# Kernel tuning notes

Hardware: AMD Instinct MI355X
Metric: run time of the kernel (lower is better)

## Reference

```python
import jax, jax.numpy as jnp
import numpy as np

N_NODES = 100000
N_EDGES = 1600000
D_IN = 128
D_OUT = 128


def setup_inputs() -> dict:
    key = jax.random.key(0)
    ks = jax.random.split(key, 6)
    x = jax.random.normal(ks[0], (N_NODES, D_IN), dtype=jnp.float32)
    edge_index = jax.random.randint(ks[1], (2, N_EDGES), 0, N_NODES, dtype=jnp.int64)
    W_l = jax.random.normal(ks[2], (D_OUT, D_IN), dtype=jnp.float32) * 0.05
    b_l = jax.random.normal(ks[3], (D_OUT,), dtype=jnp.float32) * 0.05
    W_r = jax.random.normal(ks[4], (D_OUT, D_IN), dtype=jnp.float32) * 0.05
    b_r = jax.random.normal(ks[5], (D_OUT,), dtype=jnp.float32) * 0.05
    return {"x": x, "edge_index": edge_index, "W_l": W_l, "b_l": b_l, "W_r": W_r, "b_r": b_r}


def reference(x, edge_index, W_l, b_l, W_r, b_r):
    # spmm(edge_index, x, reduce='mean'): out[row] = mean_{edges with that row} x[col]
    row = edge_index[0]
    col = edge_index[1]
    n = x.shape[0]
    agg = jax.ops.segment_sum(x[col], row, num_segments=n)  # [N, D_IN]
    deg = jax.ops.segment_sum(jnp.ones((edge_index.shape[1],), dtype=x.dtype), row, num_segments=n)
    mean = agg / jnp.maximum(deg, 1.0)[:, None]
    # lin_l(mean) + lin_r(x)
    return mean @ W_l.T + b_l + x @ W_r.T + b_r
```

## Files before the change

### kernel.cpp

```cpp
#include <hip/hip_runtime.h>

#define D 128
#define NPB 128
#define MAXBK 800
#define NBLK 256

typedef __attribute__((ext_vector_type(8))) short short8;
typedef __attribute__((ext_vector_type(4))) float f32x4;

__device__ __forceinline__ unsigned short f2bf(float f) {
    unsigned u = __float_as_uint(f);
    return (unsigned short)((u + 0x7fffu + ((u >> 16) & 1u)) >> 16);
}

__global__ void split_kernel(const float4* __restrict__ x, uint2* __restrict__ xh,
                             uint2* __restrict__ xl, int n4) {
    int i = blockIdx.x * blockDim.x + threadIdx.x;
    if (i >= n4) return;
    float4 v = x[i];
    unsigned short h0 = f2bf(v.x), h1 = f2bf(v.y), h2 = f2bf(v.z), h3 = f2bf(v.w);
    float r0 = v.x - __uint_as_float((unsigned)h0 << 16);
    float r1 = v.y - __uint_as_float((unsigned)h1 << 16);
    float r2 = v.z - __uint_as_float((unsigned)h2 << 16);
    float r3 = v.w - __uint_as_float((unsigned)h3 << 16);
    unsigned short l0 = f2bf(r0), l1 = f2bf(r1), l2 = f2bf(r2), l3 = f2bf(r3);
    uint2 hh, ll;
    hh.x = (unsigned)h0 | ((unsigned)h1 << 16);
    hh.y = (unsigned)h2 | ((unsigned)h3 << 16);
    ll.x = (unsigned)l0 | ((unsigned)l1 << 16);
    ll.y = (unsigned)l2 | ((unsigned)l3 << 16);
    xh[i] = hh;
    xl[i] = ll;
}

__global__ void prepw_kernel(const float* __restrict__ Wl_in, const float* __restrict__ bl,
                             const float* __restrict__ Wr_in, const float* __restrict__ br,
                             unsigned short* __restrict__ wh, unsigned short* __restrict__ wl,
                             float* __restrict__ bias) {
    int t = blockIdx.x * blockDim.x + threadIdx.x;
    if (t < 2 * D * D) {
        int n = t >> 7;
        int k = t & (D - 1);
        float v = (n < D) ? Wl_in[n * D + k] : Wr_in[(n - D) * D + k];
        unsigned short h = f2bf(v);
        float r = v - __uint_as_float((unsigned)h << 16);
        wh[t] = h;
        wl[t] = f2bf(r);
    }
    if (t < D) bias[t] = bl[t] + br[t];
}

__global__ __launch_bounds__(256) void hist_kernel(const int* __restrict__ ei,
                                                   int* __restrict__ cnt,
                                                   int E, int nbk, int chunk) {
    __shared__ int h[MAXBK];
    int b = blockIdx.x, t = threadIdx.x;
    for (int i = t; i < nbk; i += 256) h[i] = 0;
    __syncthreads();
    int lo = b * chunk, hi = min(E, lo + chunk);
    for (int e = lo + t; e < hi; e += 256)
        atomicAdd(&h[ei[e] >> 7], 1);
    __syncthreads();
    for (int i = t; i < nbk; i += 256) cnt[i * NBLK + b] = h[i];
}

__global__ __launch_bounds__(256) void scan_cnt_kernel(int* __restrict__ cnt,
                                                       int* __restrict__ btot) {
    int b = blockIdx.x, t = threadIdx.x;
    int lane = t & 63, w = t >> 6;
    int v = cnt[b * NBLK + t];
    int s = v;
    for (int off = 1; off < 64; off <<= 1) {
        int u = __shfl_up(s, off, 64);
        if (lane >= off) s += u;
    }
    __shared__ int wsum[4], woff[4];
    if (lane == 63) wsum[w] = s;
    __syncthreads();
    if (t == 0) {
        int run = 0;
        for (int i = 0; i < 4; ++i) { woff[i] = run; run += wsum[i]; }
        btot[b] = run;
    }
    __syncthreads();
    cnt[b * NBLK + t] = s - v + woff[w];
}

__global__ void scan_btot_kernel(const int* __restrict__ btot, int* __restrict__ bbase,
                                 int* __restrict__ row_start, int nbk, int n) {
    __shared__ int s[1024];
    int t = threadIdx.x;
    int v = (t < nbk) ? btot[t] : 0;
    s[t] = v;
    __syncthreads();
    for (int off = 1; off < 1024; off <<= 1) {
        int u = (t >= off) ? s[t - off] : 0;
        __syncthreads();
        s[t] += u;
        __syncthreads();
    }
    if (t < nbk) bbase[t] = s[t] - v;
    if (t == 1023) { bbase[nbk] = s[1023]; row_start[n] = s[1023]; }
}

__global__ __launch_bounds__(256) void scatter_kernel(const int* __restrict__ ei,
                                                      const int* __restrict__ cnt,
                                                      const int* __restrict__ bbase,
                                                      unsigned* __restrict__ pk,
                                                      int E, int nbk, int chunk) {
    __shared__ int curs[MAXBK];
    int b = blockIdx.x, t = threadIdx.x;
    for (int i = t; i < nbk; i += 256) curs[i] = bbase[i] + cnt[i * NBLK + b];
    __syncthreads();
    int lo = b * chunk, hi = min(E, lo + chunk);
    for (int e = lo + t; e < hi; e += 256) {
        int r = ei[e];
        int c = ei[E + e];
        int pos = atomicAdd(&curs[r >> 7], 1);
        pk[pos] = ((unsigned)(r & (NPB - 1)) << 17) | (unsigned)c;
    }
}

__global__ __launch_bounds__(256) void place_kernel(const int* __restrict__ bbase,
                                                    const unsigned* __restrict__ pk,
                                                    int* __restrict__ row_start,
                                                    int* __restrict__ col_sorted, int n) {
    __shared__ int hist[NPB];
    __shared__ int pre[NPB];
    int b = blockIdx.x, t = threadIdx.x;
    if (t < NPB) hist[t] = 0;
    __syncthreads();
    int s0 = bbase[b], e0 = bbase[b + 1];
    for (int i = s0 + t; i < e0; i += 256)
        atomicAdd(&hist[pk[i] >> 17], 1);
    __syncthreads();
    if (t < NPB) pre[t] = hist[t];
    __syncthreads();
    for (int off = 1; off < NPB; off <<= 1) {
        int u = (t >= off && t < NPB) ? pre[t - off] : 0;
        __syncthreads();
        if (t < NPB) pre[t] += u;
        __syncthreads();
    }
    if (t < NPB) {
        int ex = pre[t] - hist[t];
        int node = b * NPB + t;
        if (node < n) row_start[node] = s0 + ex;
        hist[t] = ex;
    }
    __syncthreads();
    for (int i = s0 + t; i < e0; i += 256) {
        unsigned p = pk[i];
        int slot = atomicAdd(&hist[p >> 17], 1);
        col_sorted[s0 + slot] = (int)(p & 0x1FFFFu);
    }
}

__global__ __launch_bounds__(256) void mm_kernel(const unsigned short* __restrict__ xh,
                                                 const unsigned short* __restrict__ xl,
                                                 const unsigned short* __restrict__ wh,
                                                 const unsigned short* __restrict__ wl,
                                                 const float* __restrict__ bias,
                                                 unsigned short* __restrict__ yl,
                                                 float* __restrict__ out, int n) {
    int w = threadIdx.x >> 6;
    int l = threadIdx.x & 63;
    int ml = l & 15;
    int kq = l >> 4;
    int m0 = blockIdx.x * 64;
    int n0 = w * 64;

    f32x4 acc[4][4];
#pragma unroll
    for (int a = 0; a < 4; ++a)
#pragma unroll
        for (int b = 0; b < 4; ++b) acc[a][b] = (f32x4){0.f, 0.f, 0.f, 0.f};

#pragma unroll
    for (int ks = 0; ks < 4; ++ks) {
        short8 Ah[4], Al[4];
#pragma unroll
        for (int mf = 0; mf < 4; ++mf) {
            int row = m0 + mf * 16 + ml;
            if (row > n - 1) row = n - 1;
            size_t off = (size_t)row * D + ks * 32 + kq * 8;
            Ah[mf] = *(const short8*)(xh + off);
            Al[mf] = *(const short8*)(xl + off);
        }
#pragma unroll
        for (int nf = 0; nf < 4; ++nf) {
            size_t boff = (size_t)(n0 + nf * 16 + ml) * D + ks * 32 + kq * 8;
            short8 Bh = *(const short8*)(wh + boff);
            short8 Bl = *(const short8*)(wl + boff);
#pragma unroll
            for (int mf = 0; mf < 4; ++mf) {
                acc[mf][nf] = __builtin_amdgcn_mfma_f32_16x16x32_bf16(Ah[mf], Bh, acc[mf][nf], 0, 0, 0);
                acc[mf][nf] = __builtin_amdgcn_mfma_f32_16x16x32_bf16(Ah[mf], Bl, acc[mf][nf], 0, 0, 0);
                acc[mf][nf] = __builtin_amdgcn_mfma_f32_16x16x32_bf16(Al[mf], Bh, acc[mf][nf], 0, 0, 0);
            }
        }
    }

    if (n0 < D) {
#pragma unroll
        for (int nf = 0; nf < 4; ++nf) {
            int col = n0 + nf * 16 + ml;
#pragma unroll
            for (int mf = 0; mf < 4; ++mf) {
                int rbase = m0 + mf * 16 + kq * 4;
#pragma unroll
                for (int r = 0; r < 4; ++r) {
                    int row = rbase + r;
                    if (row < n) yl[(size_t)row * D + col] = f2bf(acc[mf][nf][r]);
                }
            }
        }
    } else {
#pragma unroll
        for (int nf = 0; nf < 4; ++nf) {
            int col = n0 - D + nf * 16 + ml;
            float bv = bias[col];
#pragma unroll
            for (int mf = 0; mf < 4; ++mf) {
                int rbase = m0 + mf * 16 + kq * 4;
#pragma unroll
                for (int r = 0; r < 4; ++r) {
                    int row = rbase + r;
                    if (row < n) out[(size_t)row * D + col] = acc[mf][nf][r] + bv;
                }
            }
        }
    }
}

__global__ void gather_kernel(const unsigned short* __restrict__ yl,
                              const int* __restrict__ col_sorted,
                              const int* __restrict__ row_start,
                              float* __restrict__ out, int n) {
    int wave = (int)((blockIdx.x * (size_t)blockDim.x + threadIdx.x) >> 6);
    int lane = threadIdx.x & 63;
    if (wave >= n) return;
    int s = row_start[wave];
    int e = row_start[wave + 1];
    float a0 = 0.f, a1 = 0.f;
    int j = s;
    for (; j + 3 < e; j += 4) {
        int c0 = col_sorted[j], c1 = col_sorted[j + 1], c2 = col_sorted[j + 2], c3 = col_sorted[j + 3];
        unsigned v0 = *(const unsigned*)(yl + (size_t)c0 * D + 2 * lane);
        unsigned v1 = *(const unsigned*)(yl + (size_t)c1 * D + 2 * lane);
        unsigned v2 = *(const unsigned*)(yl + (size_t)c2 * D + 2 * lane);
        unsigned v3 = *(const unsigned*)(yl + (size_t)c3 * D + 2 * lane);
        a0 += __uint_as_float(v0 << 16) + __uint_as_float(v1 << 16) +
              __uint_as_float(v2 << 16) + __uint_as_float(v3 << 16);
        a1 += __uint_as_float(v0 & 0xffff0000u) + __uint_as_float(v1 & 0xffff0000u) +
              __uint_as_float(v2 & 0xffff0000u) + __uint_as_float(v3 & 0xffff0000u);
    }
    for (; j < e; ++j) {
        unsigned v = *(const unsigned*)(yl + (size_t)col_sorted[j] * D + 2 * lane);
        a0 += __uint_as_float(v << 16);
        a1 += __uint_as_float(v & 0xffff0000u);
    }
    float inv = (e > s) ? 1.0f / (float)(e - s) : 0.0f;
    float2* po = (float2*)(out + (size_t)wave * D + 2 * lane);
    float2 cur = *po;
    cur.x += a0 * inv;
    cur.y += a1 * inv;
    *po = cur;
}

extern "C" void kernel_launch(void* const* d_in, const int* in_sizes, int n_in,
                              void* d_out, int out_size, void* d_ws, size_t ws_size,
                              hipStream_t stream) {
    const float* x  = (const float*)d_in[0];
    const int*   ei = (const int*)d_in[1];
    const float* Wl = (const float*)d_in[2];
    const float* bl = (const float*)d_in[3];
    const float* Wr = (const float*)d_in[4];
    const float* br = (const float*)d_in[5];
    float* out = (float*)d_out;

    const int n = in_sizes[0] / D;
    const int E = in_sizes[1] / 2;
    const int nbk = (n + NPB - 1) / NPB;
    const int chunk = (E + NBLK - 1) / NBLK;

    char* p = (char*)d_ws;
    auto alloc = [&](size_t bytes) {
        char* r = p;
        p += (bytes + 1023) & ~(size_t)1023;
        return r;
    };
    int*   row_start  = (int*)alloc((size_t)(n + 1) * 4);
    int*   col_sorted = (int*)alloc((size_t)E * 4);
    int*   cnt        = (int*)alloc((size_t)nbk * NBLK * 4);
    int*   btot       = (int*)alloc((size_t)nbk * 4);
    int*   bbase      = (int*)alloc((size_t)(nbk + 1) * 4);
    unsigned* pk      = (unsigned*)alloc((size_t)E * 4);
    unsigned short* wh   = (unsigned short*)alloc((size_t)2 * D * D * 2);
    unsigned short* wlsp = (unsigned short*)alloc((size_t)2 * D * D * 2);
    float* bias       = (float*)alloc((size_t)D * 4);
    unsigned short* xh = (unsigned short*)alloc((size_t)n * D * 2);
    unsigned short* xl = (unsigned short*)alloc((size_t)n * D * 2);
    unsigned short* yl = (unsigned short*)alloc((size_t)n * D * 2);

    int n4 = n * D / 4;
    split_kernel<<<(n4 + 255) / 256, 256, 0, stream>>>((const float4*)x, (uint2*)xh, (uint2*)xl, n4);
    prepw_kernel<<<(2 * D * D + 255) / 256, 256, 0, stream>>>(Wl, bl, Wr, br, wh, wlsp, bias);
    hist_kernel<<<NBLK, 256, 0, stream>>>(ei, cnt, E, nbk, chunk);
    scan_cnt_kernel<<<nbk, 256, 0, stream>>>(cnt, btot);
    scan_btot_kernel<<<1, 1024, 0, stream>>>(btot, bbase, row_start, nbk, n);
    scatter_kernel<<<NBLK, 256, 0, stream>>>(ei, cnt, bbase, pk, E, nbk, chunk);
    place_kernel<<<nbk, 256, 0, stream>>>(bbase, pk, row_start, col_sorted, n);
    mm_kernel<<<(n + 63) / 64, 256, 0, stream>>>(xh, xl, wh, wlsp, bias, yl, out, n);
    gather_kernel<<<(n * 64 + 255) / 256, 256, 0, stream>>>(yl, col_sorted, row_start, out, n);
}
```

Before: 335.0 us.

## Fuse fp32-to-bf16 hi/lo split of x into matmul kernel via LDS

Removes the separate split kernel that wrote bf16 high and low copies of x to global memory. The matmul kernel now loads fp32 x tiles directly, splits them in registers, and stores them to XOR-swizzled shared memory for the MFMA operand loads. This saves one kernel launch and a full write-then-reread of two bf16 copies of x, about 100 MB of traffic. In exchange it adds 32 KB of LDS per block, which may reduce occupancy, and an extra barrier.

```diff
diff --git a/kernel.cpp b/kernel.cpp
--- a/kernel.cpp
+++ b/kernel.cpp
@@ -11,26 +11,6 @@
 __device__ __forceinline__ unsigned short f2bf(float f) {
     unsigned u = __float_as_uint(f);
     return (unsigned short)((u + 0x7fffu + ((u >> 16) & 1u)) >> 16);
-}
-
-__global__ void split_kernel(const float4* __restrict__ x, uint2* __restrict__ xh,
-                             uint2* __restrict__ xl, int n4) {
-    int i = blockIdx.x * blockDim.x + threadIdx.x;
-    if (i >= n4) return;
-    float4 v = x[i];
-    unsigned short h0 = f2bf(v.x), h1 = f2bf(v.y), h2 = f2bf(v.z), h3 = f2bf(v.w);
-    float r0 = v.x - __uint_as_float((unsigned)h0 << 16);
-    float r1 = v.y - __uint_as_float((unsigned)h1 << 16);
-    float r2 = v.z - __uint_as_float((unsigned)h2 << 16);
-    float r3 = v.w - __uint_as_float((unsigned)h3 << 16);
-    unsigned short l0 = f2bf(r0), l1 = f2bf(r1), l2 = f2bf(r2), l3 = f2bf(r3);
-    uint2 hh, ll;
-    hh.x = (unsigned)h0 | ((unsigned)h1 << 16);
-    hh.y = (unsigned)h2 | ((unsigned)h3 << 16);
-    ll.x = (unsigned)l0 | ((unsigned)l1 << 16);
-    ll.y = (unsigned)l2 | ((unsigned)l3 << 16);
-    xh[i] = hh;
-    xl[i] = ll;
 }
 
 __global__ void prepw_kernel(const float* __restrict__ Wl_in, const float* __restrict__ bl,
@@ -156,20 +136,47 @@
     }
 }
 
-__global__ __launch_bounds__(256) void mm_kernel(const unsigned short* __restrict__ xh,
-                                                 const unsigned short* __restrict__ xl,
+__global__ __launch_bounds__(256) void mm_kernel(const float* __restrict__ x,
                                                  const unsigned short* __restrict__ wh,
                                                  const unsigned short* __restrict__ wl,
                                                  const float* __restrict__ bias,
                                                  unsigned short* __restrict__ yl,
                                                  float* __restrict__ out, int n) {
-    int w = threadIdx.x >> 6;
-    int l = threadIdx.x & 63;
+    __shared__ unsigned short AhL[64 * D];
+    __shared__ unsigned short AlL[64 * D];
+    int t = threadIdx.x;
+    int w = t >> 6;
+    int l = t & 63;
     int ml = l & 15;
     int kq = l >> 4;
     int m0 = blockIdx.x * 64;
     int n0 = w * 64;
 
+#pragma unroll
+    for (int i = 0; i < 8; ++i) {
+        int f = t + (i << 8);
+        int row = f >> 5;
+        int c4 = f & 31;
+        int rg = m0 + row;
+        if (rg > n - 1) rg = n - 1;
+        float4 v = *(const float4*)(x + (size_t)rg * D + (c4 << 2));
+        unsigned short h0 = f2bf(v.x), h1 = f2bf(v.y), h2 = f2bf(v.z), h3 = f2bf(v.w);
+        float r0 = v.x - __uint_as_float((unsigned)h0 << 16);
+        float r1 = v.y - __uint_as_float((unsigned)h1 << 16);
+        float r2 = v.z - __uint_as_float((unsigned)h2 << 16);
+        float r3 = v.w - __uint_as_float((unsigned)h3 << 16);
+        uint2 hh, ll;
+        hh.x = (unsigned)h0 | ((unsigned)h1 << 16);
+        hh.y = (unsigned)h2 | ((unsigned)h3 << 16);
+        ll.x = (unsigned)f2bf(r0) | ((unsigned)f2bf(r1) << 16);
+        ll.y = (unsigned)f2bf(r2) | ((unsigned)f2bf(r3) << 16);
+        int byte = (row << 8) + (c4 << 3);
+        byte ^= (row & 7) << 4;
+        *(uint2*)((char*)AhL + byte) = hh;
+        *(uint2*)((char*)AlL + byte) = ll;
+    }
+    __syncthreads();
+
     f32x4 acc[4][4];
 #pragma unroll
     for (int a = 0; a < 4; ++a)
@@ -181,11 +188,11 @@
         short8 Ah[4], Al[4];
 #pragma unroll
         for (int mf = 0; mf < 4; ++mf) {
-            int row = m0 + mf * 16 + ml;
-            if (row > n - 1) row = n - 1;
-            size_t off = (size_t)row * D + ks * 32 + kq * 8;
-            Ah[mf] = *(const short8*)(xh + off);
-            Al[mf] = *(const short8*)(xl + off);
+            int row = mf * 16 + ml;
+            int byte = (row << 8) + (ks << 6) + (kq << 4);
+            byte ^= (row & 7) << 4;
+            Ah[mf] = *(const short8*)((const char*)AhL + byte);
+            Al[mf] = *(const short8*)((const char*)AlL + byte);
         }
 #pragma unroll
         for (int nf = 0; nf < 4; ++nf) {
@@ -299,18 +306,14 @@
     unsigned short* wh   = (unsigned short*)alloc((size_t)2 * D * D * 2);
     unsigned short* wlsp = (unsigned short*)alloc((size_t)2 * D * D * 2);
     float* bias       = (float*)alloc((size_t)D * 4);
-    unsigned short* xh = (unsigned short*)alloc((size_t)n * D * 2);
-    unsigned short* xl = (unsigned short*)alloc((size_t)n * D * 2);
     unsigned short* yl = (unsigned short*)alloc((size_t)n * D * 2);
 
-    int n4 = n * D / 4;
-    split_kernel<<<(n4 + 255) / 256, 256, 0, stream>>>((const float4*)x, (uint2*)xh, (uint2*)xl, n4);
     prepw_kernel<<<(2 * D * D + 255) / 256, 256, 0, stream>>>(Wl, bl, Wr, br, wh, wlsp, bias);
     hist_kernel<<<NBLK, 256, 0, stream>>>(ei, cnt, E, nbk, chunk);
     scan_cnt_kernel<<<nbk, 256, 0, stream>>>(cnt, btot);
     scan_btot_kernel<<<1, 1024, 0, stream>>>(btot, bbase, row_start, nbk, n);
     scatter_kernel<<<NBLK, 256, 0, stream>>>(ei, cnt, bbase, pk, E, nbk, chunk);
     place_kernel<<<nbk, 256, 0, stream>>>(bbase, pk, row_start, col_sorted, n);
-    mm_kernel<<<(n + 63) / 64, 256, 0, stream>>>(xh, xl, wh, wlsp, bias, yl, out, n);
+    mm_kernel<<<(n + 63) / 64, 256, 0, stream>>>(x, wh, wlsp, bias, yl, out, n);
     gather_kernel<<<(n * 64 + 255) / 256, 256, 0, stream>>>(yl, col_sorted, row_start, out, n);
 }
```

Result: faster. 278.7 us (-16.8%).
